# Optimization experiments

Hardware: AMD Instinct MI355X
Metric: run time of the kernel (lower is better)

Reference implementation:

```python
import jax, jax.numpy as jnp
import numpy as np

N_RAYS = 262144  # 512x512 image
N_PTS = 64       # hardcoded in original forward (reshape(-1, 64, 3))
FAR_DELTA = 1e10 # sentinel delta appended for the last sample


def setup_inputs() -> dict:
    key = jax.random.key(0)
    k1, k2, k3 = jax.random.split(key, 3)
    # non-negative densities, as a density field would produce
    density = jax.random.uniform(k1, (N_RAYS, N_PTS, 1), dtype=jnp.float32)
    # sorted depths along each ray in [2, 6] (typical near/far bounds)
    depth_values = jnp.sort(
        2.0 + 4.0 * jax.random.uniform(k2, (N_RAYS, N_PTS), dtype=jnp.float32),
        axis=-1,
    )
    rays_feature = jax.random.uniform(k3, (N_RAYS, N_PTS, 3), dtype=jnp.float32)
    return {"density": density, "depth_values": depth_values, "rays_feature": rays_feature}


def reference(density, depth_values, rays_feature):
    # deltas: consecutive depth differences, with huge sentinel for last sample
    deltas = jnp.concatenate(
        [depth_values[:, 1:] - depth_values[:, :-1],
         jnp.full_like(depth_values[:, :1], FAR_DELTA)],
        axis=-1,
    )  # (N, P)
    sigma_delta = density[..., 0] * deltas          # (N, P)
    trans_step = jnp.exp(-sigma_delta)              # per-segment transmittance e
    # exclusive cumulative product: T_0 = 1, T_i = prod_{j<i} e_j
    transmittance = jnp.concatenate(
        [jnp.ones_like(trans_step[:, :1]),
         jnp.cumprod(trans_step[:, :-1], axis=1)],
        axis=1,
    )  # (N, P)
    weights = transmittance * (1.0 - trans_step)    # (N, P)
    feature = jnp.sum(weights[..., None] * rays_feature, axis=1)  # (N, 3)
    depth = jnp.sum(weights * depth_values, axis=1)               # (N,)
    return feature, depth
```

## Files before the change

### kernel.cpp

```cpp
#include <hip/hip_runtime.h>
#include <hip/hip_bf16.h>

#define N_RAYS 262144
#define N_PTS  64
#define FAR_DELTA 1e10f
#define RAYS_PER_BLOCK 4

__global__ __launch_bounds__(256) void volume_render_kernel(
    const float* __restrict__ density,
    const float* __restrict__ depth_values,
    const float* __restrict__ rays_feature,
    float* __restrict__ out)
{
    const int wave = threadIdx.x >> 6;
    const int lane = threadIdx.x & 63;
    const int ray  = blockIdx.x * RAYS_PER_BLOCK + wave;
    if (ray >= N_RAYS) return;

    const long base = (long)ray * N_PTS;

    const float d_i  = depth_values[base + lane];
    const float sig  = density[base + lane];

    float d_next = __shfl_down(d_i, 1, 64);
    float delta  = (lane == 63) ? FAR_DELTA : (d_next - d_i);
    float sd     = sig * delta;

    float s = sd;
    #pragma unroll
    for (int off = 1; off < 64; off <<= 1) {
        float t = __shfl_up(s, off, 64);
        if (lane >= off) s += t;
    }
    float s_exc = __shfl_up(s, 1, 64);
    if (lane == 0) s_exc = 0.0f;

    const float e = __expf(-sd);
    const float w = __expf(-s_exc) * (1.0f - e);

    const float* fp = rays_feature + (long)ray * (N_PTS * 3) + lane * 3;
    float wfx = w * fp[0];
    float wfy = w * fp[1];
    float wfz = w * fp[2];
    float wd  = w * d_i;

    #pragma unroll
    for (int off = 32; off > 0; off >>= 1) {
        wfx += __shfl_xor(wfx, off, 64);
        wfy += __shfl_xor(wfy, off, 64);
        wfz += __shfl_xor(wfz, off, 64);
        wd  += __shfl_xor(wd,  off, 64);
    }

    if (lane == 0) {
        out[(long)ray * 3 + 0] = wfx;
        out[(long)ray * 3 + 1] = wfy;
        out[(long)ray * 3 + 2] = wfz;
        out[(long)N_RAYS * 3 + ray] = wd;
    }
}

extern "C" void kernel_launch(void* const* d_in, const int* in_sizes, int n_in,
                              void* d_out, int out_size, void* d_ws, size_t ws_size,
                              hipStream_t stream) {
    const float* density      = (const float*)d_in[0];
    const float* depth_values = (const float*)d_in[1];
    const float* rays_feature = (const float*)d_in[2];
    float* out = (float*)d_out;

    const int blocks = N_RAYS / RAYS_PER_BLOCK;
    volume_render_kernel<<<blocks, 256, 0, stream>>>(
        density, depth_values, rays_feature, out);
}
```

Before: 347.4 us.

## Switch to thread-per-ray with LDS-staged coalesced tiles and sequential transmittance

Replaces the wave-per-ray shuffle scan and reduction with one thread per ray that walks the samples sequentially, keeping a running transmittance product. Inputs are loaded with coalesced float4 reads into padded shared-memory tiles of 16 samples per ray. This removes the cross-lane shuffle overhead and the strided scalar feature loads. In exchange it uses 64-thread blocks, needs block-wide barriers per tile, and changes the cumulative product's rounding order.

```diff
diff --git a/kernel.cpp b/kernel.cpp
--- a/kernel.cpp
+++ b/kernel.cpp
@@ -4,60 +4,90 @@
 #define N_RAYS 262144
 #define N_PTS  64
 #define FAR_DELTA 1e10f
-#define RAYS_PER_BLOCK 4
 
-__global__ __launch_bounds__(256) void volume_render_kernel(
+#define RPB 64
+#define ST  16
+#define NT  (N_PTS/ST)
+
+#define DS_STRIDE 17
+#define FT_STRIDE 49
+
+__global__ __launch_bounds__(64) void volume_render_kernel(
     const float* __restrict__ density,
     const float* __restrict__ depth_values,
     const float* __restrict__ rays_feature,
     float* __restrict__ out)
 {
-    const int wave = threadIdx.x >> 6;
-    const int lane = threadIdx.x & 63;
-    const int ray  = blockIdx.x * RAYS_PER_BLOCK + wave;
-    if (ray >= N_RAYS) return;
+    __shared__ float s_dens[RPB * DS_STRIDE];
+    __shared__ float s_dep [RPB * DS_STRIDE];
+    __shared__ float s_feat[RPB * FT_STRIDE];
 
-    const long base = (long)ray * N_PTS;
+    const int t    = threadIdx.x;
+    const int ray0 = blockIdx.x * RPB;
 
-    const float d_i  = depth_values[base + lane];
-    const float sig  = density[base + lane];
-
-    float d_next = __shfl_down(d_i, 1, 64);
-    float delta  = (lane == 63) ? FAR_DELTA : (d_next - d_i);
-    float sd     = sig * delta;
-
-    float s = sd;
-    #pragma unroll
-    for (int off = 1; off < 64; off <<= 1) {
-        float t = __shfl_up(s, off, 64);
-        if (lane >= off) s += t;
-    }
-    float s_exc = __shfl_up(s, 1, 64);
-    if (lane == 0) s_exc = 0.0f;
-
-    const float e = __expf(-sd);
-    const float w = __expf(-s_exc) * (1.0f - e);
-
-    const float* fp = rays_feature + (long)ray * (N_PTS * 3) + lane * 3;
-    float wfx = w * fp[0];
-    float wfy = w * fp[1];
-    float wfz = w * fp[2];
-    float wd  = w * d_i;
+    float T = 1.0f;
+    float ax = 0.f, ay = 0.f, az = 0.f, ad = 0.f;
+    float sig_p = 0.f, d_p = 0.f, fx_p = 0.f, fy_p = 0.f, fz_p = 0.f;
 
     #pragma unroll
-    for (int off = 32; off > 0; off >>= 1) {
-        wfx += __shfl_xor(wfx, off, 64);
-        wfy += __shfl_xor(wfy, off, 64);
-        wfz += __shfl_xor(wfz, off, 64);
-        wd  += __shfl_xor(wd,  off, 64);
+    for (int tile = 0; tile < NT; ++tile) {
+        const int s0 = tile * ST;
+        __syncthreads();
+
+        #pragma unroll
+        for (int i = 0; i < 4; ++i) {
+            const unsigned flat = i * 64u + t;
+            const int r = flat >> 2;
+            const int q = flat & 3;
+            const size_t g = (size_t)(ray0 + r) * N_PTS + s0 + q * 4;
+            const float4 dv = *(const float4*)(density + g);
+            const float4 zv = *(const float4*)(depth_values + g);
+            float* dd = &s_dens[r * DS_STRIDE + q * 4];
+            float* zz = &s_dep [r * DS_STRIDE + q * 4];
+            dd[0] = dv.x; dd[1] = dv.y; dd[2] = dv.z; dd[3] = dv.w;
+            zz[0] = zv.x; zz[1] = zv.y; zz[2] = zv.z; zz[3] = zv.w;
+        }
+        #pragma unroll
+        for (int i = 0; i < 12; ++i) {
+            const unsigned flat = i * 64u + t;
+            const unsigned r = flat / 12u;
+            const unsigned q = flat - r * 12u;
+            const size_t g = (size_t)(ray0 + r) * (N_PTS * 3) + s0 * 3 + q * 4;
+            const float4 fv = *(const float4*)(rays_feature + g);
+            float* ff = &s_feat[r * FT_STRIDE + q * 4];
+            ff[0] = fv.x; ff[1] = fv.y; ff[2] = fv.z; ff[3] = fv.w;
+        }
+        __syncthreads();
+
+        #pragma unroll
+        for (int j = 0; j < ST; ++j) {
+            const float d  = s_dep [t * DS_STRIDE + j];
+            const float sg = s_dens[t * DS_STRIDE + j];
+            const float fx = s_feat[t * FT_STRIDE + 3 * j + 0];
+            const float fy = s_feat[t * FT_STRIDE + 3 * j + 1];
+            const float fz = s_feat[t * FT_STRIDE + 3 * j + 2];
+            if (tile > 0 || j > 0) {
+                const float delta = d - d_p;
+                const float e = __expf(-sig_p * delta);
+                const float w = T * (1.0f - e);
+                ax += w * fx_p; ay += w * fy_p; az += w * fz_p; ad += w * d_p;
+                T *= e;
+            }
+            sig_p = sg; d_p = d; fx_p = fx; fy_p = fy; fz_p = fz;
+        }
     }
 
-    if (lane == 0) {
-        out[(long)ray * 3 + 0] = wfx;
-        out[(long)ray * 3 + 1] = wfy;
-        out[(long)ray * 3 + 2] = wfz;
-        out[(long)N_RAYS * 3 + ray] = wd;
+    {
+        const float e = __expf(-sig_p * FAR_DELTA);
+        const float w = T * (1.0f - e);
+        ax += w * fx_p; ay += w * fy_p; az += w * fz_p; ad += w * d_p;
     }
+
+    const int ray = ray0 + t;
+    out[(size_t)ray * 3 + 0] = ax;
+    out[(size_t)ray * 3 + 1] = ay;
+    out[(size_t)ray * 3 + 2] = az;
+    out[(size_t)N_RAYS * 3 + ray] = ad;
 }
 
 extern "C" void kernel_launch(void* const* d_in, const int* in_sizes, int n_in,
@@ -68,7 +98,7 @@
     const float* rays_feature = (const float*)d_in[2];
     float* out = (float*)d_out;
 
-    const int blocks = N_RAYS / RAYS_PER_BLOCK;
-    volume_render_kernel<<<blocks, 256, 0, stream>>>(
+    const int blocks = N_RAYS / RPB;
+    volume_render_kernel<<<blocks, RPB, 0, stream>>>(
         density, depth_values, rays_feature, out);
 }
```

Result: slower. 365.9 us (+5.3%).

## Process each ray with four lanes of sixteen samples using vector loads

Applied to the files above, without the earlier changes.

Remaps work so that four lanes share a ray, each holding sixteen consecutive samples in registers. Loads use float4, a serial prefix sum runs within each lane, and only a two-step shuffle scan and reduction run across lanes. Weights are computed as differences of exponentials of the running optical depth instead of transmittance times (1−e). This cuts the per-sample cross-lane shuffle traffic and scalar strided loads, at the cost of more registers per thread and uncoalesced per-instruction access patterns.

```diff
diff --git a/kernel.cpp b/kernel.cpp
--- a/kernel.cpp
+++ b/kernel.cpp
@@ -4,59 +4,85 @@
 #define N_RAYS 262144
 #define N_PTS  64
 #define FAR_DELTA 1e10f
-#define RAYS_PER_BLOCK 4
+#define LPR 4
+#define SPL 16
 
-__global__ __launch_bounds__(256) void volume_render_kernel(
+__global__ __launch_bounds__(256, 4) void volume_render_kernel(
     const float* __restrict__ density,
     const float* __restrict__ depth_values,
     const float* __restrict__ rays_feature,
     float* __restrict__ out)
 {
-    const int wave = threadIdx.x >> 6;
-    const int lane = threadIdx.x & 63;
-    const int ray  = blockIdx.x * RAYS_PER_BLOCK + wave;
-    if (ray >= N_RAYS) return;
+    const int t   = threadIdx.x;
+    const int sub = t & (LPR - 1);
+    const int ray = blockIdx.x * (256 / LPR) + (t >> 2);
 
-    const long base = (long)ray * N_PTS;
+    const size_t sbase = (size_t)ray * N_PTS + sub * SPL;
 
-    const float d_i  = depth_values[base + lane];
-    const float sig  = density[base + lane];
+    float d[SPL], sd[SPL];
+    #pragma unroll
+    for (int q = 0; q < 4; ++q) {
+        const float4 dv = *(const float4*)(depth_values + sbase + q * 4);
+        d[q*4+0] = dv.x; d[q*4+1] = dv.y; d[q*4+2] = dv.z; d[q*4+3] = dv.w;
+    }
+    #pragma unroll
+    for (int q = 0; q < 4; ++q) {
+        const float4 sv = *(const float4*)(density + sbase + q * 4);
+        sd[q*4+0] = sv.x; sd[q*4+1] = sv.y; sd[q*4+2] = sv.z; sd[q*4+3] = sv.w;
+    }
 
-    float d_next = __shfl_down(d_i, 1, 64);
-    float delta  = (lane == 63) ? FAR_DELTA : (d_next - d_i);
-    float sd     = sig * delta;
-
-    float s = sd;
-    #pragma unroll
-    for (int off = 1; off < 64; off <<= 1) {
-        float t = __shfl_up(s, off, 64);
-        if (lane >= off) s += t;
-    }
-    float s_exc = __shfl_up(s, 1, 64);
-    if (lane == 0) s_exc = 0.0f;
-
-    const float e = __expf(-sd);
-    const float w = __expf(-s_exc) * (1.0f - e);
-
-    const float* fp = rays_feature + (long)ray * (N_PTS * 3) + lane * 3;
-    float wfx = w * fp[0];
-    float wfy = w * fp[1];
-    float wfz = w * fp[2];
-    float wd  = w * d_i;
+    const float d_next0 = __shfl_down(d[0], 1, 64);
 
     #pragma unroll
-    for (int off = 32; off > 0; off >>= 1) {
-        wfx += __shfl_xor(wfx, off, 64);
-        wfy += __shfl_xor(wfy, off, 64);
-        wfz += __shfl_xor(wfz, off, 64);
-        wd  += __shfl_xor(wd,  off, 64);
+    for (int i = 0; i < SPL - 1; ++i) sd[i] *= (d[i+1] - d[i]);
+    sd[SPL-1] *= (sub == LPR-1) ? FAR_DELTA : (d_next0 - d[SPL-1]);
+
+    float P[SPL];
+    P[0] = sd[0];
+    #pragma unroll
+    for (int i = 1; i < SPL; ++i) P[i] = P[i-1] + sd[i];
+
+    float s = P[SPL-1];
+    float u = __shfl_up(s, 1, 64); if (sub >= 1) s += u;
+    u       = __shfl_up(s, 2, 64); if (sub >= 2) s += u;
+    float B = __shfl_up(s, 1, 64); if (sub == 0) B = 0.0f;
+
+    float w[SPL];
+    float Xprev = __expf(-B);
+    #pragma unroll
+    for (int i = 0; i < SPL; ++i) {
+        const float Xi = __expf(-(B + P[i]));
+        w[i] = Xprev - Xi;
+        Xprev = Xi;
     }
 
-    if (lane == 0) {
-        out[(long)ray * 3 + 0] = wfx;
-        out[(long)ray * 3 + 1] = wfy;
-        out[(long)ray * 3 + 2] = wfz;
-        out[(long)N_RAYS * 3 + ray] = wd;
+    float ax = 0.f, ay = 0.f, az = 0.f, ad = 0.f;
+    #pragma unroll
+    for (int i = 0; i < SPL; ++i) ad += w[i] * d[i];
+
+    const float* fbase = rays_feature + (size_t)ray * (N_PTS * 3) + sub * (SPL * 3);
+    #pragma unroll
+    for (int g = 0; g < 4; ++g) {
+        const float4 f0 = *(const float4*)(fbase + g * 12 + 0);
+        const float4 f1 = *(const float4*)(fbase + g * 12 + 4);
+        const float4 f2 = *(const float4*)(fbase + g * 12 + 8);
+        const int i0 = g * 4;
+        ax += w[i0+0]*f0.x; ay += w[i0+0]*f0.y; az += w[i0+0]*f0.z;
+        ax += w[i0+1]*f0.w; ay += w[i0+1]*f1.x; az += w[i0+1]*f1.y;
+        ax += w[i0+2]*f1.z; ay += w[i0+2]*f1.w; az += w[i0+2]*f2.x;
+        ax += w[i0+3]*f2.y; ay += w[i0+3]*f2.z; az += w[i0+3]*f2.w;
+    }
+
+    ax += __shfl_xor(ax, 1, 64); ay += __shfl_xor(ay, 1, 64);
+    az += __shfl_xor(az, 1, 64); ad += __shfl_xor(ad, 1, 64);
+    ax += __shfl_xor(ax, 2, 64); ay += __shfl_xor(ay, 2, 64);
+    az += __shfl_xor(az, 2, 64); ad += __shfl_xor(ad, 2, 64);
+
+    if (sub == 0) {
+        out[(size_t)ray * 3 + 0] = ax;
+        out[(size_t)ray * 3 + 1] = ay;
+        out[(size_t)ray * 3 + 2] = az;
+        out[(size_t)N_RAYS * 3 + ray] = ad;
     }
 }
 
@@ -68,7 +94,7 @@
     const float* rays_feature = (const float*)d_in[2];
     float* out = (float*)d_out;
 
-    const int blocks = N_RAYS / RAYS_PER_BLOCK;
+    const int blocks = N_RAYS / (256 / LPR);
     volume_render_kernel<<<blocks, 256, 0, stream>>>(
         density, depth_values, rays_feature, out);
 }
```

Result: slower. 374.5 us (+7.8%).
